# Optimization experiments

Measured on AMD Instinct MI355X. Metric: run time of the kernel, lower is better.

## Reference

```python
import jax, jax.numpy as jnp
import numpy as np

HID = 256
VOC = 50257
N_E_SH = 2
N_E_SP = 2
N_MB = 4
B, S = 8, 512
LN_EPS = 1e-3  # keras LayerNormalization default epsilon
STD = 0.02


def setup_inputs() -> dict:
    key = jax.random.key(0)
    ks = jax.random.split(key, 10)
    x = jax.random.normal(ks[0], (B, S, HID), dtype=jnp.float32)
    # labels drawn in [1, VOC) so the `labels > 0` mask keeps every token (static shape)
    labels = jax.random.randint(ks[1], (B, S), 1, VOC, dtype=jnp.int32)
    xb = jax.random.randint(ks[2], (B, S), 0, N_MB + 1, dtype=jnp.int32)
    W_sh = jax.random.normal(ks[3], (N_E_SH, HID, HID), dtype=jnp.float32) * STD
    b_sh = jax.random.normal(ks[4], (N_E_SH, HID), dtype=jnp.float32) * STD
    W_sp = jax.random.normal(ks[5], (N_MB * N_E_SP, HID, HID), dtype=jnp.float32) * STD
    b_sp = jax.random.normal(ks[6], (N_MB * N_E_SP, HID), dtype=jnp.float32) * STD
    w_gates = jax.random.normal(ks[7], (N_MB, HID, N_E_SH + N_E_SP), dtype=jnp.float32) * STD
    vocab_bias = jax.random.normal(ks[8], (VOC,), dtype=jnp.float32) * STD
    emb = jax.random.normal(ks[9], (VOC, HID), dtype=jnp.float32) * STD  # tied_to.weights[0]
    ln_gamma = jnp.ones((HID,), dtype=jnp.float32)
    ln_beta = jnp.zeros((HID,), dtype=jnp.float32)
    return {"x": x, "labels": labels, "xb": xb, "W_sh": W_sh, "b_sh": b_sh,
            "W_sp": W_sp, "b_sp": b_sp, "w_gates": w_gates,
            "vocab_bias": vocab_bias, "emb": emb,
            "ln_gamma": ln_gamma, "ln_beta": ln_beta}


def _layernorm(h, gamma, beta):
    mu = jnp.mean(h, axis=-1, keepdims=True)
    var = jnp.mean(jnp.square(h - mu), axis=-1, keepdims=True)
    return gamma * (h - mu) * jax.lax.rsqrt(var + LN_EPS) + beta


def reference(x, labels, xb, W_sh, b_sh, W_sp, b_sp, w_gates, vocab_bias, emb, ln_gamma, ln_beta):
    xf = x.reshape(-1, HID)          # [N, H]
    lf = labels.reshape(-1)          # [N], all > 0 => mask gather is identity
    xbf = xb.reshape(-1)             # [N]

    # shared + branch-specific experts: [e, N, H]
    sh = jnp.einsum('nd,edh->enh', xf, W_sh) + b_sh[:, None, :]
    sp = jnp.einsum('nd,edh->enh', xf, W_sp) + b_sp[:, None, :]
    sp = sp.reshape(N_MB, N_E_SP, -1, HID)                       # [t, e_sp, N, H]
    sh_b = jnp.broadcast_to(sh[None], (N_MB, N_E_SH, sh.shape[1], HID))
    merge = jnp.concatenate([sh_b, sp], axis=1)                  # [t, e, N, H]

    gates = jax.nn.softmax(jnp.einsum('nd,tde->tne', xf, w_gates), axis=-1)  # [t, N, e]
    out = jnp.einsum('tend,tne->tnd', merge, gates)              # [t, N, H]

    outputs = jnp.concatenate([jnp.zeros_like(xf)[None], out], axis=0)  # [t+1, N, H]
    oh = jax.nn.one_hot(xbf, N_MB + 1, dtype=jnp.float32)        # [N, t+1]
    e_out = jnp.einsum('tnd,nt->nd', outputs, oh)                # [N, H]

    e_out = _layernorm(e_out, ln_gamma, ln_beta) + xf

    logits = e_out @ emb.T + vocab_bias                          # [N, VOC]
    logp = jax.nn.log_softmax(logits, axis=-1)
    loss = -jnp.take_along_axis(logp, lf[:, None], axis=-1)[:, 0]  # [N]
    prob = jnp.exp(logp)
    return prob, loss
```

## Files before the change

### kernel.cpp

```cpp
#include <hip/hip_runtime.h>

#define HID 256
#define VOC 50257
#define NTOK 4096
#define NCT3 393
#define CG 8
#define TN 128
#define LN_EPS 1e-3f
#define PROB_ELEMS 205852672

typedef __attribute__((ext_vector_type(8))) short bf16x8;
typedef __attribute__((ext_vector_type(4))) float f32x4;
typedef __attribute__((ext_vector_type(16))) float f32x16;

__device__ inline unsigned short f2bf(float f) {
    unsigned int u = __builtin_bit_cast(unsigned int, f);
    unsigned int r = u + 0x7FFFu + ((u >> 16) & 1u);
    return (unsigned short)(r >> 16);
}
__device__ inline float bf2f(unsigned short b) {
    unsigned int u = ((unsigned int)b) << 16;
    return __builtin_bit_cast(float, u);
}

__global__ void conv_f32_bf16(const float* __restrict__ src,
                              unsigned short* __restrict__ dst, int n4) {
    int i = blockIdx.x * blockDim.x + threadIdx.x;
    int stride = gridDim.x * blockDim.x;
    for (; i < n4; i += stride) {
        float4 v = reinterpret_cast<const float4*>(src)[i];
        ushort4 o;
        o.x = f2bf(v.x); o.y = f2bf(v.y); o.z = f2bf(v.z); o.w = f2bf(v.w);
        reinterpret_cast<ushort4*>(dst)[i] = o;
    }
}

__global__ __launch_bounds__(256) void wt_transpose(
    const float* __restrict__ Wsh, const float* __restrict__ Wsp,
    unsigned short* __restrict__ Wtbf) {
    __shared__ float t[64][65];
    int gcol0 = blockIdx.x * 64;
    int k0 = blockIdx.y * 64;
    int e = gcol0 >> 8, h0 = gcol0 & 255;
    const float* Wp = (e < 2) ? (Wsh + e * 65536) : (Wsp + (e - 2) * 65536);
    int tid = threadIdx.x;
#pragma unroll
    for (int i = 0; i < 16; ++i) {
        int id = tid + i * 256;
        int k = id >> 6, h = id & 63;
        t[k][h] = Wp[(k0 + k) * 256 + h0 + h];
    }
    __syncthreads();
#pragma unroll
    for (int i = 0; i < 4; ++i) {
        int id = tid + i * 256;
        int h = id >> 4, kq = id & 15;
        ushort4 o;
        o.x = f2bf(t[kq * 4 + 0][h]); o.y = f2bf(t[kq * 4 + 1][h]);
        o.z = f2bf(t[kq * 4 + 2][h]); o.w = f2bf(t[kq * 4 + 3][h]);
        *reinterpret_cast<ushort4*>(Wtbf + (size_t)(gcol0 + h) * 256 + k0 + kq * 4) = o;
    }
}

__global__ __launch_bounds__(256) void expert_gemm(
    const unsigned short* __restrict__ xbf,
    const unsigned short* __restrict__ Wtbf,
    const float* __restrict__ bsh, const float* __restrict__ bsp,
    float* __restrict__ cexp) {
    __shared__ unsigned short sA[64 * 256];
    __shared__ unsigned short sB[128 * 256];
    int bid = blockIdx.x;
    int rt = bid & 63;
    int ct = bid >> 6;
    int row0 = rt * 64, col0 = ct * 128;
    int tid = threadIdx.x;

#pragma unroll
    for (int i = 0; i < 8; ++i) {
        int id = tid + i * 256;
        int r = id >> 5, c = id & 31;
        bf16x8 v = *reinterpret_cast<const bf16x8*>(xbf + (row0 + r) * 256 + c * 8);
        *reinterpret_cast<bf16x8*>(sA + r * 256 + ((c ^ (r & 7)) * 8)) = v;
    }
#pragma unroll
    for (int i = 0; i < 16; ++i) {
        int id = tid + i * 256;
        int j = id >> 5, c = id & 31;
        bf16x8 v = *reinterpret_cast<const bf16x8*>(Wtbf + (size_t)(col0 + j) * 256 + c * 8);
        *reinterpret_cast<bf16x8*>(sB + j * 256 + ((c ^ (j & 7)) * 8)) = v;
    }
    __syncthreads();

    int lane = tid & 63, wave = tid >> 6;
    int wcol = wave * 32;
    int lrow = lane & 15, g = lane >> 4;
    f32x4 zero4 = {0.f, 0.f, 0.f, 0.f};
    f32x4 acc[4][2];
#pragma unroll
    for (int mf = 0; mf < 4; ++mf)
#pragma unroll
        for (int nf = 0; nf < 2; ++nf) acc[mf][nf] = zero4;

#pragma unroll
    for (int ks = 0; ks < 8; ++ks) {
        int kc = ks * 4 + g;
        bf16x8 a[4], b[2];
#pragma unroll
        for (int mf = 0; mf < 4; ++mf) {
            int r = mf * 16 + lrow;
            a[mf] = *reinterpret_cast<const bf16x8*>(sA + r * 256 + ((kc ^ (r & 7)) * 8));
        }
#pragma unroll
        for (int nf = 0; nf < 2; ++nf) {
            int j = wcol + nf * 16 + lrow;
            b[nf] = *reinterpret_cast<const bf16x8*>(sB + j * 256 + ((kc ^ (j & 7)) * 8));
        }
#pragma unroll
        for (int mf = 0; mf < 4; ++mf)
#pragma unroll
            for (int nf = 0; nf < 2; ++nf)
                acc[mf][nf] = __builtin_amdgcn_mfma_f32_16x16x32_bf16(a[mf], b[nf], acc[mf][nf], 0, 0, 0);
    }

#pragma unroll
    for (int nf = 0; nf < 2; ++nf) {
        int col = col0 + wcol + nf * 16 + lrow;
        int e = col >> 8, h = col & 255;
        float bias = (e < 2) ? bsh[e * 256 + h] : bsp[(e - 2) * 256 + h];
#pragma unroll
        for (int mf = 0; mf < 4; ++mf)
#pragma unroll
            for (int r = 0; r < 4; ++r) {
                int row = row0 + mf * 16 + g * 4 + r;
                cexp[(size_t)row * 2560 + col] = acc[mf][nf][r] + bias;
            }
    }
}

__global__ __launch_bounds__(256) void combine_ln(
    const float* __restrict__ x, const int* __restrict__ xb,
    const float* __restrict__ wg, const float* __restrict__ cexp,
    const float* __restrict__ gamma, const float* __restrict__ beta,
    unsigned short* __restrict__ ebf) {
    __shared__ float sx[256];
    __shared__ float sg[4];
    __shared__ float rs[4], rq[4];
    int n = blockIdx.x, h = threadIdx.x;
    float xv = x[n * 256 + h];
    sx[h] = xv;
    __syncthreads();
    int xbn = xb[n];
    float eo;
    if (xbn == 0) {
        eo = beta[h] + xv;
    } else {
        int t = xbn - 1;
        int wv = h >> 6, lane = h & 63;
        float p = 0.f;
        const float* wgt = wg + t * 1024;
#pragma unroll
        for (int i = 0; i < 4; ++i) {
            int d = lane * 4 + i;
            p += sx[d] * wgt[d * 4 + wv];
        }
#pragma unroll
        for (int off = 32; off; off >>= 1) p += __shfl_down(p, off);
        if (lane == 0) sg[wv] = p;
        __syncthreads();
        float g0 = sg[0], g1 = sg[1], g2 = sg[2], g3 = sg[3];
        float mx = fmaxf(fmaxf(g0, g1), fmaxf(g2, g3));
        float e0 = __expf(g0 - mx), e1 = __expf(g1 - mx);
        float e2 = __expf(g2 - mx), e3 = __expf(g3 - mx);
        float inv = 1.f / (e0 + e1 + e2 + e3);
        const float* cr = cexp + (size_t)n * 2560;
        float o = (e0 * cr[h] + e1 * cr[256 + h] +
                   e2 * cr[512 + t * 512 + h] + e3 * cr[768 + t * 512 + h]) * inv;
        float s = o, q = o * o;
#pragma unroll
        for (int off = 32; off; off >>= 1) { s += __shfl_down(s, off); q += __shfl_down(q, off); }
        if (lane == 0) { rs[wv] = s; rq[wv] = q; }
        __syncthreads();
        float mu = (rs[0] + rs[1] + rs[2] + rs[3]) * (1.f / 256.f);
        float ex2 = (rq[0] + rq[1] + rq[2] + rq[3]) * (1.f / 256.f);
        float var = ex2 - mu * mu;
        eo = gamma[h] * (o - mu) * rsqrtf(var + LN_EPS) + beta[h] + xv;
    }
    ebf[n * 256 + h] = f2bf(eo);
}

template <int PASS>
__global__ __launch_bounds__(512, 2) void big_gemm(
    const unsigned short* __restrict__ ebf,
    const unsigned short* __restrict__ embbf,
    const float* __restrict__ vbias,
    float* __restrict__ psum,
    const float* __restrict__ denom,
    float* __restrict__ prob) {
    __shared__ unsigned short sB[2][TN * 256];

    int bid = blockIdx.x;
    int rt = bid >> 3;
    int cg = bid & 7;
    int row0 = rt * 128;
    int tid = threadIdx.x;
    int wave = tid >> 6, lane = tid & 63;
    int l31 = lane & 31, hi = lane >> 5;
    int wr = wave >> 2, wc = wave & 3;
    int nmy = (NCT3 - cg + CG - 1) / CG;

    bf16x8 a[2][16];
    {
        const unsigned short* ab =
            ebf + (size_t)(row0 + wr * 64 + l31) * 256 + hi * 8;
#pragma unroll
        for (int mf = 0; mf < 2; ++mf)
#pragma unroll
            for (int ks = 0; ks < 16; ++ks)
                a[mf][ks] = *reinterpret_cast<const bf16x8*>(ab + mf * 32 * 256 + ks * 16);
    }

    auto stage = [&](int ct, int buf) {
        int col0 = ct * TN;
#pragma unroll
        for (int i = 0; i < 8; ++i) {
            int col = i * 16 + wave * 2 + hi;
            int gcol = col0 + col; if (gcol >= VOC) gcol = VOC - 1;
            const unsigned short* src =
                embbf + (size_t)gcol * 256 + ((l31 ^ (col & 7)) * 8);
            unsigned short* dst = (unsigned short*)sB[buf] + (size_t)(i * 512 + wave * 64) * 8;
            __builtin_amdgcn_global_load_lds(
                (const __attribute__((address_space(1))) void*)src,
                (__attribute__((address_space(3))) void*)dst, 16, 0, 0);
        }
    };

    stage(cg, 0);
    asm volatile("s_waitcnt vmcnt(0)" ::: "memory");
    __syncthreads();

    float invd[2][16];
    if (PASS == 1) {
#pragma unroll
        for (int mf = 0; mf < 2; ++mf)
#pragma unroll
            for (int r = 0; r < 16; ++r) {
                int row = row0 + wr * 64 + mf * 32 + (r & 3) + 8 * (r >> 2) + 4 * hi;
                invd[mf][r] = 1.f / denom[row];
            }
    }
    float es[2][16];
    if (PASS == 0) {
#pragma unroll
        for (int mf = 0; mf < 2; ++mf)
#pragma unroll
            for (int r = 0; r < 16; ++r) es[mf][r] = 0.f;
    }

    f32x16 zz = {0.f,0.f,0.f,0.f,0.f,0.f,0.f,0.f,0.f,0.f,0.f,0.f,0.f,0.f,0.f,0.f};

    for (int it = 0; it < nmy; ++it) {
        int ct = cg + it * CG;
        if (it + 1 < nmy) stage(ct + CG, (it + 1) & 1);

        int gc = ct * TN + wc * 32 + l31;
        float bvb = (gc < VOC) ? vbias[gc] : -1e4f;

        const unsigned short* sBc = (const unsigned short*)sB[it & 1];
        int bcol = wc * 32 + l31;
        f32x16 c0 = zz, c1 = zz;
#pragma unroll
        for (int ks = 0; ks < 16; ++ks) {
            int kc = ks * 2 + hi;
            bf16x8 b = *reinterpret_cast<const bf16x8*>(
                sBc + bcol * 256 + ((kc ^ (bcol & 7)) * 8));
            c0 = __builtin_amdgcn_mfma_f32_32x32x16_bf16(a[0][ks], b, c0, 0, 0, 0);
            c1 = __builtin_amdgcn_mfma_f32_32x32x16_bf16(a[1][ks], b, c1, 0, 0, 0);
        }

        asm volatile("s_waitcnt vmcnt(0)" ::: "memory");
        __syncthreads();

        if (PASS == 0) {
#pragma unroll
            for (int r = 0; r < 16; ++r) {
                es[0][r] += __expf(c0[r] + bvb);
                es[1][r] += __expf(c1[r] + bvb);
            }
        } else {
            if (gc < VOC) {
#pragma unroll
                for (int r = 0; r < 16; ++r) {
                    int rowr = row0 + wr * 64 + (r & 3) + 8 * (r >> 2) + 4 * hi;
                    prob[(size_t)rowr * VOC + gc] = __expf(c0[r] + bvb) * invd[0][r];
                    prob[(size_t)(rowr + 32) * VOC + gc] = __expf(c1[r] + bvb) * invd[1][r];
                }
            }
        }
    }

    if (PASS == 0) {
#pragma unroll
        for (int mf = 0; mf < 2; ++mf)
#pragma unroll
            for (int r = 0; r < 16; ++r) {
                float v = es[mf][r];
#pragma unroll
                for (int off = 1; off < 32; off <<= 1) v += __shfl_xor(v, off);
                if (l31 == 0) {
                    int row = row0 + wr * 64 + mf * 32 + (r & 3) + 8 * (r >> 2) + 4 * hi;
                    psum[(size_t)row * 32 + cg * 4 + wc] = v;
                }
            }
    }
}

__global__ __launch_bounds__(64) void finalize_k(
    const float* __restrict__ psum,
    const unsigned short* __restrict__ ebf, const unsigned short* __restrict__ embbf,
    const float* __restrict__ vbias, const int* __restrict__ labels,
    float* __restrict__ denom, float* __restrict__ loss) {
    int n = blockIdx.x, lane = threadIdx.x;
    float s = (lane < 32) ? psum[(size_t)n * 32 + lane] : 0.f;
#pragma unroll
    for (int off = 1; off < 32; off <<= 1) s += __shfl_xor(s, off);
    int lf = labels[n];
    const unsigned short* ev = ebf + n * 256;
    const unsigned short* mv = embbf + (size_t)lf * 256;
    float p = 0.f;
#pragma unroll
    for (int i = 0; i < 4; ++i) p += bf2f(ev[lane * 4 + i]) * bf2f(mv[lane * 4 + i]);
#pragma unroll
    for (int off = 1; off < 64; off <<= 1) p += __shfl_xor(p, off);
    if (lane == 0) {
        denom[n] = s;
        loss[n] = logf(s) - (p + vbias[lf]);
    }
}

extern "C" void kernel_launch(void* const* d_in, const int* in_sizes, int n_in,
                              void* d_out, int out_size, void* d_ws, size_t ws_size,
                              hipStream_t stream) {
    const float* x      = (const float*)d_in[0];
    const int*   labels = (const int*)d_in[1];
    const int*   xb     = (const int*)d_in[2];
    const float* Wsh    = (const float*)d_in[3];
    const float* bsh    = (const float*)d_in[4];
    const float* Wsp    = (const float*)d_in[5];
    const float* bsp    = (const float*)d_in[6];
    const float* wg     = (const float*)d_in[7];
    const float* vbias  = (const float*)d_in[8];
    const float* emb    = (const float*)d_in[9];
    const float* gamma  = (const float*)d_in[10];
    const float* beta   = (const float*)d_in[11];

    char* ws = (char*)d_ws;
    unsigned short* xbf   = (unsigned short*)(ws + 0);
    unsigned short* embbf = (unsigned short*)(ws + 2097152);
    unsigned short* Wtbf  = (unsigned short*)(ws + 27828736);
    float* cexp           = (float*)(ws + 29360128);
    unsigned short* ebf   = (unsigned short*)(ws + 71303168);
    float* psum           = (float*)(ws + 73400320);
    float* denom          = (float*)(ws + 73924608);

    float* prob = (float*)d_out;
    float* loss = prob + PROB_ELEMS;

    conv_f32_bf16<<<dim3(512), dim3(256), 0, stream>>>(x, xbf, NTOK * HID / 4);
    conv_f32_bf16<<<dim3(2048), dim3(256), 0, stream>>>(emb, embbf, VOC * HID / 4);
    wt_transpose<<<dim3(40, 4), dim3(256), 0, stream>>>(Wsh, Wsp, Wtbf);
    expert_gemm<<<dim3(64 * 20), dim3(256), 0, stream>>>(xbf, Wtbf, bsh, bsp, cexp);
    combine_ln<<<dim3(NTOK), dim3(256), 0, stream>>>(x, xb, wg, cexp, gamma, beta, ebf);
    big_gemm<0><<<dim3(256), dim3(512), 0, stream>>>(ebf, embbf, vbias, psum, nullptr, nullptr);
    finalize_k<<<dim3(NTOK), dim3(64), 0, stream>>>(psum, ebf, embbf, vbias, labels, denom, loss);
    big_gemm<1><<<dim3(256), dim3(512), 0, stream>>>(ebf, embbf, vbias, nullptr, denom, prob);
}
```

Baseline: 542.9 us.

## Load vocab embedding fragments directly from global memory, drop LDS staging

Removes the double-buffered LDS staging of the embedding tile in both vocab passes. Each wave now reads its B fragments straight from global memory (L2-cached), which eliminates the per-iteration barrier and waitcnt. The probability output is written with nontemporal stores to keep the large output from polluting cache. The trade-off is that the four waves sharing a row tile no longer share one LDS copy, and global load latency is now exposed in the MFMA loop unless the partial unroll hides it.

```diff
diff --git a/kernel.cpp b/kernel.cpp
--- a/kernel.cpp
+++ b/kernel.cpp
@@ -5,7 +5,6 @@
 #define NTOK 4096
 #define NCT3 393
 #define CG 8
-#define TN 128
 #define LN_EPS 1e-3f
 #define PROB_ELEMS 205852672
 
@@ -189,15 +188,13 @@
 }
 
 template <int PASS>
-__global__ __launch_bounds__(512, 2) void big_gemm(
+__global__ __launch_bounds__(512, 2) void vocab_pass(
     const unsigned short* __restrict__ ebf,
     const unsigned short* __restrict__ embbf,
     const float* __restrict__ vbias,
     float* __restrict__ psum,
     const float* __restrict__ denom,
     float* __restrict__ prob) {
-    __shared__ unsigned short sB[2][TN * 256];
-
     int bid = blockIdx.x;
     int rt = bid >> 3;
     int cg = bid & 7;
@@ -219,25 +216,6 @@
                 a[mf][ks] = *reinterpret_cast<const bf16x8*>(ab + mf * 32 * 256 + ks * 16);
     }
 
-    auto stage = [&](int ct, int buf) {
-        int col0 = ct * TN;
-#pragma unroll
-        for (int i = 0; i < 8; ++i) {
-            int col = i * 16 + wave * 2 + hi;
-            int gcol = col0 + col; if (gcol >= VOC) gcol = VOC - 1;
-            const unsigned short* src =
-                embbf + (size_t)gcol * 256 + ((l31 ^ (col & 7)) * 8);
-            unsigned short* dst = (unsigned short*)sB[buf] + (size_t)(i * 512 + wave * 64) * 8;
-            __builtin_amdgcn_global_load_lds(
-                (const __attribute__((address_space(1))) void*)src,
-                (__attribute__((address_space(3))) void*)dst, 16, 0, 0);
-        }
-    };
-
-    stage(cg, 0);
-    asm volatile("s_waitcnt vmcnt(0)" ::: "memory");
-    __syncthreads();
-
     float invd[2][16];
     if (PASS == 1) {
 #pragma unroll
@@ -260,25 +238,20 @@
 
     for (int it = 0; it < nmy; ++it) {
         int ct = cg + it * CG;
-        if (it + 1 < nmy) stage(ct + CG, (it + 1) & 1);
-
-        int gc = ct * TN + wc * 32 + l31;
-        float bvb = (gc < VOC) ? vbias[gc] : -1e4f;
-
-        const unsigned short* sBc = (const unsigned short*)sB[it & 1];
-        int bcol = wc * 32 + l31;
+        int gc = ct * 128 + wc * 32 + l31;
+        int gcc = (gc < VOC) ? gc : (VOC - 1);
+        const unsigned short* bp = embbf + (size_t)gcc * 256 + hi * 8;
+        float bvb;
+        if (PASS == 0) bvb = (gc < VOC) ? vbias[gc] : -1e4f;
+        else           bvb = vbias[gcc];
+
         f32x16 c0 = zz, c1 = zz;
-#pragma unroll
+#pragma unroll 8
         for (int ks = 0; ks < 16; ++ks) {
-            int kc = ks * 2 + hi;
-            bf16x8 b = *reinterpret_cast<const bf16x8*>(
-                sBc + bcol * 256 + ((kc ^ (bcol & 7)) * 8));
+            bf16x8 b = *reinterpret_cast<const bf16x8*>(bp + ks * 16);
             c0 = __builtin_amdgcn_mfma_f32_32x32x16_bf16(a[0][ks], b, c0, 0, 0, 0);
             c1 = __builtin_amdgcn_mfma_f32_32x32x16_bf16(a[1][ks], b, c1, 0, 0, 0);
         }
-
-        asm volatile("s_waitcnt vmcnt(0)" ::: "memory");
-        __syncthreads();
 
         if (PASS == 0) {
 #pragma unroll
@@ -291,8 +264,10 @@
 #pragma unroll
                 for (int r = 0; r < 16; ++r) {
                     int rowr = row0 + wr * 64 + (r & 3) + 8 * (r >> 2) + 4 * hi;
-                    prob[(size_t)rowr * VOC + gc] = __expf(c0[r] + bvb) * invd[0][r];
-                    prob[(size_t)(rowr + 32) * VOC + gc] = __expf(c1[r] + bvb) * invd[1][r];
+                    __builtin_nontemporal_store(__expf(c0[r] + bvb) * invd[0][r],
+                                                prob + (size_t)rowr * VOC + gc);
+                    __builtin_nontemporal_store(__expf(c1[r] + bvb) * invd[1][r],
+                                                prob + (size_t)(rowr + 32) * VOC + gc);
                 }
             }
         }
@@ -370,7 +345,7 @@
     wt_transpose<<<dim3(40, 4), dim3(256), 0, stream>>>(Wsh, Wsp, Wtbf);
     expert_gemm<<<dim3(64 * 20), dim3(256), 0, stream>>>(xbf, Wtbf, bsh, bsp, cexp);
     combine_ln<<<dim3(NTOK), dim3(256), 0, stream>>>(x, xb, wg, cexp, gamma, beta, ebf);
-    big_gemm<0><<<dim3(256), dim3(512), 0, stream>>>(ebf, embbf, vbias, psum, nullptr, nullptr);
+    vocab_pass<0><<<dim3(256), dim3(512), 0, stream>>>(ebf, embbf, vbias, psum, nullptr, nullptr);
     finalize_k<<<dim3(NTOK), dim3(64), 0, stream>>>(psum, ebf, embbf, vbias, labels, denom, loss);
-    big_gemm<1><<<dim3(256), dim3(512), 0, stream>>>(ebf, embbf, vbias, nullptr, denom, prob);
-}
+    vocab_pass<1><<<dim3(256), dim3(512), 0, stream>>>(ebf, embbf, vbias, nullptr, denom, prob);
+}
```

Result: slower. 1.516 ms (+179.2%).

## Defer prob stores one tile and fuse x bf16 conversion into expert GEMM

Applied to the files above, without the earlier changes.

In the second big GEMM pass, the computed probabilities are buffered in registers and written out during the next iteration. The wait before the barrier becomes vmcnt(32) instead of a full drain, so outstanding prob stores overlap the next tile's MFMAs and staging loads, and __syncthreads becomes a raw s_barrier. The separate x-to-bf16 conversion kernel is removed by converting fp32 x while loading it into shared memory in expert_gemm. The cost is extra registers for the deferred accumulators, and the partial vmcnt count must still cover the LDS staging loads.

```diff
diff --git a/kernel.cpp b/kernel.cpp
--- a/kernel.cpp
+++ b/kernel.cpp
@@ -63,7 +63,7 @@
 }
 
 __global__ __launch_bounds__(256) void expert_gemm(
-    const unsigned short* __restrict__ xbf,
+    const float* __restrict__ x,
     const unsigned short* __restrict__ Wtbf,
     const float* __restrict__ bsh, const float* __restrict__ bsp,
     float* __restrict__ cexp) {
@@ -79,8 +79,15 @@
     for (int i = 0; i < 8; ++i) {
         int id = tid + i * 256;
         int r = id >> 5, c = id & 31;
-        bf16x8 v = *reinterpret_cast<const bf16x8*>(xbf + (row0 + r) * 256 + c * 8);
-        *reinterpret_cast<bf16x8*>(sA + r * 256 + ((c ^ (r & 7)) * 8)) = v;
+        const float* xr = x + (size_t)(row0 + r) * 256 + c * 8;
+        float4 v0 = *reinterpret_cast<const float4*>(xr);
+        float4 v1 = *reinterpret_cast<const float4*>(xr + 4);
+        bf16x8 o;
+        o[0] = (short)f2bf(v0.x); o[1] = (short)f2bf(v0.y);
+        o[2] = (short)f2bf(v0.z); o[3] = (short)f2bf(v0.w);
+        o[4] = (short)f2bf(v1.x); o[5] = (short)f2bf(v1.y);
+        o[6] = (short)f2bf(v1.z); o[7] = (short)f2bf(v1.w);
+        *reinterpret_cast<bf16x8*>(sA + r * 256 + ((c ^ (r & 7)) * 8)) = o;
     }
 #pragma unroll
     for (int i = 0; i < 16; ++i) {
@@ -236,7 +243,7 @@
 
     stage(cg, 0);
     asm volatile("s_waitcnt vmcnt(0)" ::: "memory");
-    __syncthreads();
+    __builtin_amdgcn_s_barrier();
 
     float invd[2][16];
     if (PASS == 1) {
@@ -257,10 +264,24 @@
     }
 
     f32x16 zz = {0.f,0.f,0.f,0.f,0.f,0.f,0.f,0.f,0.f,0.f,0.f,0.f,0.f,0.f,0.f,0.f};
+    f32x16 c0p = zz, c1p = zz;
+    int gcp = VOC;
 
     for (int it = 0; it < nmy; ++it) {
         int ct = cg + it * CG;
         if (it + 1 < nmy) stage(ct + CG, (it + 1) & 1);
+
+        if (PASS == 1) {
+            asm volatile("" ::: "memory");
+            if (gcp < VOC) {
+#pragma unroll
+                for (int r = 0; r < 16; ++r) {
+                    int rowr = row0 + wr * 64 + (r & 3) + 8 * (r >> 2) + 4 * hi;
+                    prob[(size_t)rowr * VOC + gcp] = c0p[r];
+                    prob[(size_t)(rowr + 32) * VOC + gcp] = c1p[r];
+                }
+            }
+        }
 
         int gc = ct * TN + wc * 32 + l31;
         float bvb = (gc < VOC) ? vbias[gc] : -1e4f;
@@ -277,8 +298,9 @@
             c1 = __builtin_amdgcn_mfma_f32_32x32x16_bf16(a[1][ks], b, c1, 0, 0, 0);
         }
 
-        asm volatile("s_waitcnt vmcnt(0)" ::: "memory");
-        __syncthreads();
+        if (PASS == 0) asm volatile("s_waitcnt vmcnt(0)" ::: "memory");
+        else           asm volatile("s_waitcnt vmcnt(32)" ::: "memory");
+        __builtin_amdgcn_s_barrier();
 
         if (PASS == 0) {
 #pragma unroll
@@ -287,14 +309,12 @@
                 es[1][r] += __expf(c1[r] + bvb);
             }
         } else {
-            if (gc < VOC) {
-#pragma unroll
-                for (int r = 0; r < 16; ++r) {
-                    int rowr = row0 + wr * 64 + (r & 3) + 8 * (r >> 2) + 4 * hi;
-                    prob[(size_t)rowr * VOC + gc] = __expf(c0[r] + bvb) * invd[0][r];
-                    prob[(size_t)(rowr + 32) * VOC + gc] = __expf(c1[r] + bvb) * invd[1][r];
-                }
-            }
+#pragma unroll
+            for (int r = 0; r < 16; ++r) {
+                c0p[r] = __expf(c0[r] + bvb) * invd[0][r];
+                c1p[r] = __expf(c1[r] + bvb) * invd[1][r];
+            }
+            gcp = gc;
         }
     }
 
@@ -311,6 +331,15 @@
                     psum[(size_t)row * 32 + cg * 4 + wc] = v;
                 }
             }
+    } else {
+        if (gcp < VOC) {
+#pragma unroll
+            for (int r = 0; r < 16; ++r) {
+                int rowr = row0 + wr * 64 + (r & 3) + 8 * (r >> 2) + 4 * hi;
+                prob[(size_t)rowr * VOC + gcp] = c0p[r];
+                prob[(size_t)(rowr + 32) * VOC + gcp] = c1p[r];
+            }
+        }
     }
 }
 
@@ -354,7 +383,6 @@
     const float* beta   = (const float*)d_in[11];
 
     char* ws = (char*)d_ws;
-    unsigned short* xbf   = (unsigned short*)(ws + 0);
     unsigned short* embbf = (unsigned short*)(ws + 2097152);
     unsigned short* Wtbf  = (unsigned short*)(ws + 27828736);
     float* cexp           = (float*)(ws + 29360128);
@@ -365,10 +393,9 @@
     float* prob = (float*)d_out;
     float* loss = prob + PROB_ELEMS;
 
-    conv_f32_bf16<<<dim3(512), dim3(256), 0, stream>>>(x, xbf, NTOK * HID / 4);
     conv_f32_bf16<<<dim3(2048), dim3(256), 0, stream>>>(emb, embbf, VOC * HID / 4);
     wt_transpose<<<dim3(40, 4), dim3(256), 0, stream>>>(Wsh, Wsp, Wtbf);
-    expert_gemm<<<dim3(64 * 20), dim3(256), 0, stream>>>(xbf, Wtbf, bsh, bsp, cexp);
+    expert_gemm<<<dim3(64 * 20), dim3(256), 0, stream>>>(x, Wtbf, bsh, bsp, cexp);
     combine_ln<<<dim3(NTOK), dim3(256), 0, stream>>>(x, xb, wg, cexp, gamma, beta, ebf);
     big_gemm<0><<<dim3(256), dim3(512), 0, stream>>>(ebf, embbf, vbias, psum, nullptr, nullptr);
     finalize_k<<<dim3(NTOK), dim3(64), 0, stream>>>(psum, ebf, embbf, vbias, labels, denom, loss);
```

New measurement: 656.8 us. 1.21x slower.
